# Optimization experiments

Hardware: AMD Instinct MI355X
Metric: run time of the kernel (lower is better)

## Reference

```python
import jax, jax.numpy as jnp
import numpy as np

B, T, D, M = 32, 2048, 128, 256   # batch, seq_len, pitch vocab d, encoder_output_dim m
FILTERS = [256, 256, 256]
TAU = 1.0                          # gumbel_temperature
ALPHA_INV = 1.0 / (D * 100)        # W init value: 1/alpha, alpha = d*100


def causal_dilated_conv(x, w, b, dilation):
    """x: [B,T,Cin], w: [K,Cin,Cout], causal left padding."""
    k = w.shape[0]
    pad = (k - 1) * dilation
    y = jax.lax.conv_general_dilated(
        x, w, window_strides=(1,), padding=[(pad, 0)],
        rhs_dilation=(dilation,),
        dimension_numbers=('NWC', 'WIO', 'NWC'))
    return y + b


def slow_weight_model(batch, w0, b0, w1, b1, w2, b2, w_out, b_out):
    """DilatedConvBlock: stack of causal dilated convs (relu) + 1x1 readout to m logits."""
    h = jax.nn.relu(causal_dilated_conv(batch, w0, b0, dilation=1))
    h = jax.nn.relu(causal_dilated_conv(h, w1, b1, dilation=2))
    h = jax.nn.relu(causal_dilated_conv(h, w2, b2, dilation=4))
    return causal_dilated_conv(h, w_out, b_out, dilation=1)  # [B,T,M] logits


def setup_inputs() -> dict:
    key = jax.random.key(0)
    ks = jax.random.split(key, 9)
    def glorot(k, shape):
        fan_in = np.prod(shape[:-1])
        return (jax.random.normal(k, shape, jnp.float32) / np.sqrt(fan_in)).astype(jnp.float32)
    return {
        'batch': jax.random.uniform(ks[0], (B, T, D), jnp.float32),
        'w0': glorot(ks[1], (2, D, FILTERS[0])), 'b0': jnp.zeros((FILTERS[0],), jnp.float32),
        'w1': glorot(ks[2], (2, FILTERS[0], FILTERS[1])), 'b1': jnp.zeros((FILTERS[1],), jnp.float32),
        'w2': glorot(ks[3], (2, FILTERS[1], FILTERS[2])), 'b2': jnp.zeros((FILTERS[2],), jnp.float32),
        'w_out': glorot(ks[4], (1, FILTERS[2], M)), 'b_out': jnp.zeros((M,), jnp.float32),
    }


def reference(batch, w0, b0, w1, b1, w2, b2, w_out, b_out):
    logits = slow_weight_model(batch, w0, b0, w1, b1, w2, b2, w_out, b_out)  # [B,T,M]
    # short_term_method == 'softmax_normalize_after'
    h_src = jax.nn.softmax(logits / TAU, axis=2)  # [B,T,M]
    s_tar = batch                                  # [B,T,D]
    W0 = jnp.full((B, M, D), ALPHA_INV, jnp.float32)

    def step(W, hs):
        h, s = hs                                              # [B,M], [B,D]
        num = jnp.einsum('bm,bmd->bd', h, W)                   # readout
        prob = num / jnp.sum(num, axis=-1, keepdims=True)      # normalize-after
        W_new = W + h[:, :, None] * s[:, None, :]              # outer-product fast-weight update
        return W_new, prob

    W_final, probs = jax.lax.scan(
        step, W0, (jnp.swapaxes(h_src, 0, 1), jnp.swapaxes(s_tar, 0, 1)))
    probs = jnp.swapaxes(probs, 0, 1)  # [B,T,D]
    return probs, W_final
```

## Files before the change

kernel.cpp:

```cpp
#include <hip/hip_runtime.h>

using u16 = unsigned short;
using u32 = unsigned int;
using short8 = __attribute__((ext_vector_type(8))) short;
using short4v = __attribute__((ext_vector_type(4))) short;
using bf16x8 = __attribute__((ext_vector_type(8))) __bf16;
using f32x4 = __attribute__((ext_vector_type(4))) float;

#define ALPHA_INV (1.0f / (128.0f * 100.0f))

__device__ __forceinline__ u32 swz(u32 off, u32 row) { return off ^ ((row & 7u) << 4); }

__device__ __forceinline__ u16 f2bf(float x) {
  u32 u = __float_as_uint(x);
  u32 r = u + 0x7fffu + ((u >> 16) & 1u);
  return (u16)(r >> 16);
}

__device__ __forceinline__ float bf2f(u16 x) {
  u32 u = ((u32)x) << 16;
  return __uint_as_float(u);
}

__device__ __forceinline__ f32x4 mfma(bf16x8 a, bf16x8 b, f32x4 c) {
  return __builtin_amdgcn_mfma_f32_16x16x32_bf16(a, b, c, 0, 0, 0);
}

__device__ __forceinline__ void gl16(const void* g, void* l) {
  __builtin_amdgcn_global_load_lds(
      (const __attribute__((address_space(1))) unsigned int*)g,
      (__attribute__((address_space(3))) unsigned int*)l, 16, 0, 0);
}

__global__ __launch_bounds__(256) void prep(
    const float* __restrict__ batch,
    const float* __restrict__ w0, const float* __restrict__ w1,
    const float* __restrict__ w2, const float* __restrict__ wo,
    u16* __restrict__ o0, u16* __restrict__ o1,
    u16* __restrict__ o2, u16* __restrict__ o3,
    u16* __restrict__ ST) {
  __shared__ u16 L[64 * 129];
  int blk = blockIdx.x;
  if (blk < 1536) {
    const float* w; u16* o; int cin;
    if (blk < 256)       { w = w0; o = o0; cin = 128; }
    else if (blk < 768)  { w = w1; o = o1; cin = 256; blk -= 256; }
    else if (blk < 1280) { w = w2; o = o2; cin = 256; blk -= 768; }
    else                 { w = wo; o = o3; cin = 256; blk -= 1280; }
    int idx = blk * 256 + threadIdx.x;
    int row = idx >> 8, n = idx & 255;
    int tap = row / cin, c = row - tap * cin;
    int kc = c >> 6, ci = c & 63;
    u32 sb = (u32)(ci * 2) ^ ((u32)(n & 7) << 4);
    o[((size_t)tap * 256 + n) * cin + kc * 64 + (sb >> 1)] = f2bf(w[idx]);
    return;
  }
  blk -= 1536;
  const int tid = threadIdx.x;
  const int t0 = (blk & 31) * 64;
  const int b = blk >> 5;
  const float* src = batch + ((size_t)b * 2048 + t0) * 128;
#pragma unroll
  for (int it = 0; it < 4; ++it) {
    int s = tid + it * 256;
    int t = s >> 4, c8 = s & 15;
    float4 v0 = *(const float4*)(src + t * 128 + c8 * 8);
    float4 v1 = *(const float4*)(src + t * 128 + c8 * 8 + 4);
    u16* p = &L[t * 129 + c8 * 8];
    p[0] = f2bf(v0.x); p[1] = f2bf(v0.y); p[2] = f2bf(v0.z); p[3] = f2bf(v0.w);
    p[4] = f2bf(v1.x); p[5] = f2bf(v1.y); p[6] = f2bf(v1.z); p[7] = f2bf(v1.w);
  }
  __syncthreads();
  u16* dst = ST + (size_t)b * 128 * 2048 + t0;
#pragma unroll
  for (int it = 0; it < 4; ++it) {
    int s = tid + it * 256;
    int oct = s & 7, d = s >> 3;
    short8 v;
#pragma unroll
    for (int j = 0; j < 8; ++j) v[j] = (short)L[(oct * 8 + j) * 129 + d];
    *(short8*)(dst + (size_t)d * 2048 + oct * 8) = v;
  }
}

__global__ __launch_bounds__(512) void conv_first(
    const float* __restrict__ in, const u16* __restrict__ wt,
    const float* __restrict__ bias, u16* __restrict__ out) {
  constexpr int CIN = 128, BN = 256;
  __shared__ alignas(16) u16 Al[128 * 64];
  __shared__ alignas(16) u16 Bl[256 * 64];

  const int tid = threadIdx.x;
  const int wid = tid >> 6, lane = tid & 63;
  const int wr = wid >> 2, wc = wid & 3;
  const int lg = lane >> 4, lq = lane & 15;
  const int row0 = blockIdx.x * 128;
  const int tloc0 = row0 & 2047;

  f32x4 acc[4][4];
#pragma unroll
  for (int i = 0; i < 4; ++i)
#pragma unroll
    for (int j = 0; j < 4; ++j) acc[i][j] = (f32x4)0.0f;

#pragma unroll
  for (int tap = 0; tap < 2; ++tap) {
    const int shift = 1 - tap;
#pragma unroll
    for (int kc = 0; kc < 2; ++kc) {
#pragma unroll
      for (int it = 0; it < 2; ++it) {
        int gi = tid + it * 512;
        int r = gi >> 3, cg = gi & 7;
        short8 v = (short8)0;
        if (!(tloc0 == 0 && r < shift)) {
          const float* src = in + (size_t)(row0 + r - shift) * CIN + kc * 64 + cg * 8;
          float4 a = *(const float4*)src;
          float4 b2 = *(const float4*)(src + 4);
          v[0] = (short)f2bf(a.x);  v[1] = (short)f2bf(a.y);
          v[2] = (short)f2bf(a.z);  v[3] = (short)f2bf(a.w);
          v[4] = (short)f2bf(b2.x); v[5] = (short)f2bf(b2.y);
          v[6] = (short)f2bf(b2.z); v[7] = (short)f2bf(b2.w);
        }
        *(short8*)((char*)Al + swz(r * 128 + cg * 16, (u32)(r - shift + 8))) = v;
      }
      {
        const u16* wtb = wt + ((size_t)(tap * 256)) * CIN + kc * 64;
#pragma unroll
        for (int it = 0; it < 4; ++it) {
          int gi = tid + it * 512;
          int n = gi >> 3, cg = gi & 7;
          gl16(wtb + (size_t)n * CIN + cg * 8, (char*)Bl + it * 8192 + wid * 1024);
        }
      }
      __syncthreads();
#pragma unroll
      for (int ks = 0; ks < 2; ++ks) {
        bf16x8 af[4], bfr[4];
#pragma unroll
        for (int mi = 0; mi < 4; ++mi) {
          int r = wr * 64 + mi * 16 + lq;
          af[mi] = *(const bf16x8*)((const char*)Al +
                                    swz(r * 128 + ks * 64 + lg * 16, (u32)(r - shift + 8)));
        }
#pragma unroll
        for (int ni = 0; ni < 4; ++ni) {
          int n = wc * 64 + ni * 16 + lq;
          bfr[ni] = *(const bf16x8*)((const char*)Bl + swz(n * 128 + ks * 64 + lg * 16, n));
        }
#pragma unroll
        for (int mi = 0; mi < 4; ++mi)
#pragma unroll
          for (int ni = 0; ni < 4; ++ni)
            acc[mi][ni] = mfma(af[mi], bfr[ni], acc[mi][ni]);
      }
      __syncthreads();
    }
  }

  float bcol[4];
#pragma unroll
  for (int ni = 0; ni < 4; ++ni) bcol[ni] = bias[wc * 64 + ni * 16 + lq];
#pragma unroll
  for (int mi = 0; mi < 4; ++mi)
#pragma unroll
    for (int ni = 0; ni < 4; ++ni)
#pragma unroll
      for (int rr = 0; rr < 4; ++rr) {
        float v = fmaxf(acc[mi][ni][rr] + bcol[ni], 0.0f);
        int row = row0 + wr * 64 + mi * 16 + lg * 4 + rr;
        int col = wc * 64 + ni * 16 + lq;
        int ci = col & 63;
        u32 sb = (u32)(ci * 2) ^ ((u32)(row & 7) << 4);
        out[(size_t)row * BN + wc * 64 + (sb >> 1)] = f2bf(v);
      }
}

template <int DIL>
__global__ __launch_bounds__(512) void conv_mid(
    const u16* __restrict__ in, const u16* __restrict__ wt,
    const float* __restrict__ bias, u16* __restrict__ out) {
  constexpr int CIN = 256, BN = 256;
  __shared__ alignas(16) u16 Al[3][136 * 64];
  __shared__ alignas(16) u16 Bl[3][256 * 64];

  const int tid = threadIdx.x;
  const int wid = tid >> 6, lane = tid & 63;
  const int wr = wid >> 2, wc = wid & 3;
  const int lg = lane >> 4, lq = lane & 15;
  const int row0 = blockIdx.x * 128;
  const int tloc0 = row0 & 2047;

  f32x4 acc[4][4];
#pragma unroll
  for (int i = 0; i < 4; ++i)
#pragma unroll
    for (int j = 0; j < 4; ++j) acc[i][j] = (f32x4)0.0f;

#define STAGE_MID(BUF, KC, TAP)                                                          \
  {                                                                                      \
    _Pragma("unroll") for (int p = 0; p < 2; ++p) {                                      \
      int gi = tid + p * 512;                                                            \
      gl16(in + (size_t)(row0 - DIL + (gi >> 3)) * CIN + (KC)*64 + (gi & 7) * 8,         \
           (char*)Al[BUF] + p * 8192 + wid * 1024);                                      \
    }                                                                                    \
    if (wid == 0)                                                                        \
      gl16(in + (size_t)(row0 - DIL + 128 + (lane >> 3)) * CIN + (KC)*64 + (lane & 7) * 8,\
           (char*)Al[BUF] + 16384);                                                      \
    const u16* wtb = wt + (size_t)(TAP)*256 * CIN + (KC)*64;                             \
    _Pragma("unroll") for (int p = 0; p < 4; ++p) {                                      \
      int gi = tid + p * 512;                                                            \
      gl16(wtb + (size_t)(gi >> 3) * CIN + (gi & 7) * 8,                                 \
           (char*)Bl[BUF] + p * 8192 + wid * 1024);                                      \
    }                                                                                    \
  }

  STAGE_MID(0, 0, 0);
  STAGE_MID(1, 0, 1);
  if (wid == 0)
    asm volatile("s_waitcnt vmcnt(7)" ::: "memory");
  else
    asm volatile("s_waitcnt vmcnt(6)" ::: "memory");
  __builtin_amdgcn_s_barrier();

#pragma unroll
  for (int it8 = 0; it8 < 8; ++it8) {
    const int buf = it8 % 3;
    const int tap = it8 & 1;
    if (tap == 0 && tloc0 == 0) {
      if (tid < DIL * 8) *(short8*)((char*)Al[buf] + tid * 16) = (short8)0;
      asm volatile("s_waitcnt lgkmcnt(0)" ::: "memory");
      __builtin_amdgcn_s_barrier();
    }
#pragma unroll
    for (int ks = 0; ks < 2; ++ks) {
      bf16x8 af[4], bfr[4];
#pragma unroll
      for (int mi = 0; mi < 4; ++mi) {
        int r = wr * 64 + mi * 16 + lq;
        if (tap == 0)
          af[mi] = *(const bf16x8*)((const char*)Al[buf] +
                                    swz(r * 128 + ks * 64 + lg * 16, (u32)(r - DIL + 8)));
        else
          af[mi] = *(const bf16x8*)((const char*)Al[buf] +
                                    swz((r + DIL) * 128 + ks * 64 + lg * 16, (u32)(r + 8)));
      }
#pragma unroll
      for (int ni = 0; ni < 4; ++ni) {
        int n = wc * 64 + ni * 16 + lq;
        bfr[ni] = *(const bf16x8*)((const char*)Bl[buf] + swz(n * 128 + ks * 64 + lg * 16, n));
      }
#pragma unroll
      for (int mi = 0; mi < 4; ++mi)
#pragma unroll
        for (int ni = 0; ni < 4; ++ni)
          acc[mi][ni] = mfma(af[mi], bfr[ni], acc[mi][ni]);
    }
    if (it8 < 6) {
      STAGE_MID((it8 + 2) % 3, (it8 + 2) >> 1, (it8 + 2) & 1);
    }
    if (it8 < 7) {
      if (it8 < 6) {
        if (wid == 0)
          asm volatile("s_waitcnt vmcnt(7)" ::: "memory");
        else
          asm volatile("s_waitcnt vmcnt(6)" ::: "memory");
      } else {
        asm volatile("s_waitcnt vmcnt(0)" ::: "memory");
      }
      __builtin_amdgcn_s_barrier();
    }
  }
#undef STAGE_MID

  float bcol[4];
#pragma unroll
  for (int ni = 0; ni < 4; ++ni) bcol[ni] = bias[wc * 64 + ni * 16 + lq];
#pragma unroll
  for (int mi = 0; mi < 4; ++mi)
#pragma unroll
    for (int ni = 0; ni < 4; ++ni)
#pragma unroll
      for (int rr = 0; rr < 4; ++rr) {
        float v = fmaxf(acc[mi][ni][rr] + bcol[ni], 0.0f);
        int row = row0 + wr * 64 + mi * 16 + lg * 4 + rr;
        int col = wc * 64 + ni * 16 + lq;
        int ci = col & 63;
        u32 sb = (u32)(ci * 2) ^ ((u32)(row & 7) << 4);
        out[(size_t)row * BN + wc * 64 + (sb >> 1)] = f2bf(v);
      }
}

__global__ __launch_bounds__(512) void conv_last(
    const u16* __restrict__ in, const u16* __restrict__ wt,
    const float* __restrict__ bias, u16* __restrict__ out) {
  constexpr int CIN = 256, BN = 256;
  __shared__ alignas(16) u16 Al[3][128 * 64];
  __shared__ alignas(16) u16 Bl[3][256 * 64];
  __shared__ float redA[4][128];
  __shared__ float redB[4][128];

  const int tid = threadIdx.x;
  const int wid = tid >> 6, lane = tid & 63;
  const int wr = wid >> 2, wc = wid & 3;
  const int lg = lane >> 4, lq = lane & 15;
  const int row0 = blockIdx.x * 128;

  f32x4 acc[4][4];
#pragma unroll
  for (int i = 0; i < 4; ++i)
#pragma unroll
    for (int j = 0; j < 4; ++j) acc[i][j] = (f32x4)0.0f;

#define STAGE_LAST(BUF, KC)                                                              \
  {                                                                                      \
    _Pragma("unroll") for (int p = 0; p < 2; ++p) {                                      \
      int gi = tid + p * 512;                                                            \
      gl16(in + (size_t)(row0 + (gi >> 3)) * CIN + (KC)*64 + (gi & 7) * 8,               \
           (char*)Al[BUF] + p * 8192 + wid * 1024);                                      \
    }                                                                                    \
    const u16* wtb = wt + (KC)*64;                                                       \
    _Pragma("unroll") for (int p = 0; p < 4; ++p) {                                      \
      int gi = tid + p * 512;                                                            \
      gl16(wtb + (size_t)(gi >> 3) * CIN + (gi & 7) * 8,                                 \
           (char*)Bl[BUF] + p * 8192 + wid * 1024);                                      \
    }                                                                                    \
  }

  STAGE_LAST(0, 0);
  STAGE_LAST(1, 1);
  asm volatile("s_waitcnt vmcnt(6)" ::: "memory");
  __builtin_amdgcn_s_barrier();

#pragma unroll
  for (int it4 = 0; it4 < 4; ++it4) {
    const int buf = it4 % 3;
#pragma unroll
    for (int ks = 0; ks < 2; ++ks) {
      bf16x8 af[4], bfr[4];
#pragma unroll
      for (int mi = 0; mi < 4; ++mi) {
        int r = wr * 64 + mi * 16 + lq;
        af[mi] = *(const bf16x8*)((const char*)Al[buf] +
                                  swz(r * 128 + ks * 64 + lg * 16, (u32)(r + 8)));
      }
#pragma unroll
      for (int ni = 0; ni < 4; ++ni) {
        int n = wc * 64 + ni * 16 + lq;
        bfr[ni] = *(const bf16x8*)((const char*)Bl[buf] + swz(n * 128 + ks * 64 + lg * 16, n));
      }
#pragma unroll
      for (int mi = 0; mi < 4; ++mi)
#pragma unroll
        for (int ni = 0; ni < 4; ++ni)
          acc[mi][ni] = mfma(af[mi], bfr[ni], acc[mi][ni]);
    }
    if (it4 < 2) {
      STAGE_LAST((it4 + 2) % 3, it4 + 2);
    }
    if (it4 < 3) {
      if (it4 < 2)
        asm volatile("s_waitcnt vmcnt(6)" ::: "memory");
      else
        asm volatile("s_waitcnt vmcnt(0)" ::: "memory");
      __builtin_amdgcn_s_barrier();
    }
  }
#undef STAGE_LAST
  __syncthreads();

  float bcol[4];
#pragma unroll
  for (int ni = 0; ni < 4; ++ni) bcol[ni] = bias[wc * 64 + ni * 16 + lq];
#pragma unroll
  for (int mi = 0; mi < 4; ++mi)
#pragma unroll
    for (int ni = 0; ni < 4; ++ni)
#pragma unroll
      for (int rr = 0; rr < 4; ++rr) acc[mi][ni][rr] += bcol[ni];

  float tmx[4][4];
#pragma unroll
  for (int mi = 0; mi < 4; ++mi)
#pragma unroll
    for (int rr = 0; rr < 4; ++rr) {
      float v = fmaxf(fmaxf(acc[mi][0][rr], acc[mi][1][rr]),
                      fmaxf(acc[mi][2][rr], acc[mi][3][rr]));
#pragma unroll
      for (int off = 1; off < 16; off <<= 1) v = fmaxf(v, __shfl_xor(v, off));
      if (lq == 0) redA[wc][wr * 64 + mi * 16 + lg * 4 + rr] = v;
    }
  __syncthreads();
#pragma unroll
  for (int mi = 0; mi < 4; ++mi)
#pragma unroll
    for (int rr = 0; rr < 4; ++rr) {
      int rb = wr * 64 + mi * 16 + lg * 4 + rr;
      tmx[mi][rr] = fmaxf(fmaxf(redA[0][rb], redA[1][rb]),
                          fmaxf(redA[2][rb], redA[3][rb]));
    }
#pragma unroll
  for (int mi = 0; mi < 4; ++mi)
#pragma unroll
    for (int rr = 0; rr < 4; ++rr) {
      float s = 0.0f;
#pragma unroll
      for (int ni = 0; ni < 4; ++ni) {
        float p = __expf(acc[mi][ni][rr] - tmx[mi][rr]);
        acc[mi][ni][rr] = p;
        s += p;
      }
#pragma unroll
      for (int off = 1; off < 16; off <<= 1) s += __shfl_xor(s, off);
      if (lq == 0) redB[wc][wr * 64 + mi * 16 + lg * 4 + rr] = s;
    }
  __syncthreads();
#pragma unroll
  for (int mi = 0; mi < 4; ++mi)
#pragma unroll
    for (int rr = 0; rr < 4; ++rr) {
      int rb = wr * 64 + mi * 16 + lg * 4 + rr;
      float inv = 1.0f / (redB[0][rb] + redB[1][rb] + redB[2][rb] + redB[3][rb]);
      int row = row0 + rb;
#pragma unroll
      for (int ni = 0; ni < 4; ++ni) {
        int col = wc * 64 + ni * 16 + lq;
        out[(size_t)row * BN + col] = f2bf(acc[mi][ni][rr] * inv);
      }
    }
}

__global__ __launch_bounds__(512) void gchunk(
    const u16* __restrict__ H, const u16* __restrict__ ST,
    u16* __restrict__ G0, u16* __restrict__ G1) {
  constexpr int M = 256, T = 2048;
  __shared__ alignas(16) u16 Hl[128 * 128];
  __shared__ alignas(16) u16 Sl[128 * 128];
  const int tid = threadIdx.x;
  const int wid = tid >> 6, lane = tid & 63;
  const int dg = wid >> 2, mg = wid & 3;
  const int lg = lane >> 4, lq = lane & 15;
  const int b = blockIdx.x, mh = blockIdx.y, j = blockIdx.z;
  u16* G = (mh == 0 ? G0 : G1);

#pragma unroll
  for (int it = 0; it < 4; ++it) {
    int s = tid + it * 512;
    int t = s >> 4, c8 = s & 15;
    short8 v = *(const short8*)(H + ((size_t)b * T + j * 128 + t) * M + mh * 128 + c8 * 8);
#pragma unroll
    for (int jj = 0; jj < 8; ++jj) {
      int ml = c8 * 8 + jj;
      *(u16*)((char*)Hl + swz(ml * 256 + t * 2, ml)) = (u16)v[jj];
    }
  }
#pragma unroll
  for (int it = 0; it < 4; ++it) {
    int s = tid + it * 512;
    int d = s >> 4, c8 = s & 15;
    *(short8*)((char*)Sl + swz(d * 256 + c8 * 16, d)) =
        *(const short8*)(ST + ((size_t)b * 128 + d) * T + j * 128 + c8 * 8);
  }
  __syncthreads();

  f32x4 acc[4][2];
#pragma unroll
  for (int di = 0; di < 4; ++di)
#pragma unroll
    for (int mi = 0; mi < 2; ++mi) acc[di][mi] = (f32x4)0.0f;

#pragma unroll
  for (int ks = 0; ks < 4; ++ks) {
    bf16x8 sfrag[4];
#pragma unroll
    for (int di = 0; di < 4; ++di) {
      int d = dg * 64 + di * 16 + lq;
      sfrag[di] = *(const bf16x8*)((const char*)Sl + swz(d * 256 + ks * 64 + lg * 16, d));
    }
#pragma unroll
    for (int mi = 0; mi < 2; ++mi) {
      int ml = mg * 32 + mi * 16 + lq;
      bf16x8 hfrag =
          *(const bf16x8*)((const char*)Hl + swz(ml * 256 + ks * 64 + lg * 16, ml));
#pragma unroll
      for (int di = 0; di < 4; ++di) acc[di][mi] = mfma(sfrag[di], hfrag, acc[di][mi]);
    }
  }

  u16* Gj = G + (((size_t)b * 16 + j) << 14);
#pragma unroll
  for (int di = 0; di < 4; ++di)
#pragma unroll
    for (int mi = 0; mi < 2; ++mi)
#pragma unroll
      for (int rr = 0; rr < 4; ++rr) {
        int d = dg * 64 + di * 16 + lg * 4 + rr;
        int ml = mg * 32 + mi * 16 + lq;
        Gj[d * 128 + ml] = f2bf(acc[di][mi][rr]);
      }
}

__global__ __launch_bounds__(256) void prefix_wfin(
    u16* __restrict__ G0, u16* __restrict__ G1, float* __restrict__ wfin) {
  __shared__ float Wl[16][132];
  const int b = blockIdx.x, mh = blockIdx.y, ds = blockIdx.z;
  u16* G = mh ? G1 : G0;
  const int tid = threadIdx.x;
  const int mo = tid & 15, dg = tid >> 4;
  const int d = ds * 16 + dg;
  size_t base = (((size_t)b * 16) << 14) + d * 128 + mo * 8;
  float acc[8];
#pragma unroll
  for (int k = 0; k < 8; ++k) acc[k] = ALPHA_INV;
  for (int j = 0; j < 16; ++j) {
    u16* p = G + base + ((size_t)j << 14);
    short8 g = *(short8*)p;
    short8 c;
#pragma unroll
    for (int k = 0; k < 8; ++k) c[k] = (short)f2bf(acc[k]);
    *(short8*)p = c;
#pragma unroll
    for (int k = 0; k < 8; ++k) acc[k] += bf2f((u16)g[k]);
  }
#pragma unroll
  for (int k = 0; k < 8; ++k) Wl[dg][mo * 8 + k] = acc[k];
  __syncthreads();
  const int ml = tid >> 1, dq = tid & 1;
  const int dl0 = dq * 8;
  float* dst = wfin + ((size_t)b * 256 + mh * 128 + ml) * 128 + ds * 16 + dl0;
  float4 v0 = make_float4(Wl[dl0][ml], Wl[dl0 + 1][ml], Wl[dl0 + 2][ml], Wl[dl0 + 3][ml]);
  float4 v1 = make_float4(Wl[dl0 + 4][ml], Wl[dl0 + 5][ml], Wl[dl0 + 6][ml], Wl[dl0 + 7][ml]);
  *(float4*)dst = v0;
  *(float4*)(dst + 4) = v1;
}

__global__ __launch_bounds__(512) void attn_chunk(
    const u16* __restrict__ H, const u16* __restrict__ ST,
    const u16* __restrict__ C0, const u16* __restrict__ C1,
    float* __restrict__ out) {
  constexpr int M = 256, D = 128, T = 2048;
  __shared__ alignas(16) u16 Hi[128 * 256];
  __shared__ alignas(16) u16 Sl[128 * 128];
  __shared__ alignas(16) u16 Ct[128 * 128];

  const int tid = threadIdx.x;
  const int wid = tid >> 6, lane = tid & 63;
  const int lg = lane >> 4, lq = lane & 15;
  const int b = blockIdx.x, i = blockIdx.y;
  const size_t hrow0 = (size_t)b * T + i * 128;
  const size_t coff = ((size_t)b * 16 + i) * (128 * 128);

  bf16x8 aq[8];
  {
    const u16* qrow = H + (hrow0 + wid * 16 + lq) * M;
#pragma unroll
    for (int ks = 0; ks < 8; ++ks) aq[ks] = *(const bf16x8*)(qrow + ks * 32 + lg * 8);
  }

  short8 ct1r[4];
#pragma unroll
  for (int it = 0; it < 4; ++it) {
    int s = tid + it * 512;
    int d = s >> 4, c8 = s & 15;
    ct1r[it] = *(const short8*)(C1 + coff + d * 128 + c8 * 8);
  }

  {
    int r = wid * 16 + lq;
#pragma unroll
    for (int ks = 0; ks < 8; ++ks)
      *(short8*)((char*)Hi + swz(r * 512 + ks * 64 + lg * 16, r)) =
          __builtin_bit_cast(short8, aq[ks]);
  }
#pragma unroll
  for (int it = 0; it < 4; ++it) {
    int s = tid + it * 512;
    int d = s >> 4, c8 = s & 15;
    *(short8*)((char*)Sl + swz(d * 256 + c8 * 16, d)) =
        *(const short8*)(ST + ((size_t)b * D + d) * T + i * 128 + c8 * 8);
  }
#pragma unroll
  for (int it = 0; it < 4; ++it) {
    int s = tid + it * 512;
    int d = s >> 4, c8 = s & 15;
    *(short8*)((char*)Ct + swz(d * 256 + c8 * 16, d)) = *(const short8*)(C0 + coff + d * 128 + c8 * 8);
  }
  __syncthreads();

  f32x4 accO[8];
#pragma unroll
  for (int df = 0; df < 8; ++df) accO[df] = (f32x4)0.0f;
#pragma unroll
  for (int ks = 0; ks < 4; ++ks)
#pragma unroll
    for (int df = 0; df < 8; ++df) {
      int d = df * 16 + lq;
      bf16x8 bf = *(const bf16x8*)((const char*)Ct + swz(d * 256 + ks * 64 + lg * 16, d));
      accO[df] = mfma(aq[ks], bf, accO[df]);
    }
  f32x4 accP[8];
#pragma unroll
  for (int cf = 0; cf < 8; ++cf) accP[cf] = (f32x4)0.0f;
#pragma unroll
  for (int ks = 0; ks < 8; ++ks)
#pragma unroll
    for (int cf = 0; cf < 8; ++cf) {
      int tt = cf * 16 + lq;
      bf16x8 bf = *(const bf16x8*)((const char*)Hi + swz(tt * 512 + ks * 64 + lg * 16, tt));
      accP[cf] = mfma(aq[ks], bf, accP[cf]);
    }
  __syncthreads();

#pragma unroll
  for (int it = 0; it < 4; ++it) {
    int s = tid + it * 512;
    int d = s >> 4, c8 = s & 15;
    *(short8*)((char*)Ct + swz(d * 256 + c8 * 16, d)) = ct1r[it];
  }
  char* Pw = (char*)Hi + wid * 4096;
#pragma unroll
  for (int cf = 0; cf < 8; ++cf)
#pragma unroll
    for (int rr = 0; rr < 4; ++rr) {
      int ql = lg * 4 + rr;
      int tl = cf * 16 + lq;
      float v = accP[cf][rr];
      if (tl >= wid * 16 + ql) v = 0.0f;
      *(u16*)(Pw + swz(ql * 256 + tl * 2, ql)) = f2bf(v);
    }
  __syncthreads();

#pragma unroll
  for (int ks = 0; ks < 4; ++ks)
#pragma unroll
    for (int df = 0; df < 8; ++df) {
      int d = df * 16 + lq;
      bf16x8 bf = *(const bf16x8*)((const char*)Ct + swz(d * 256 + ks * 64 + lg * 16, d));
      accO[df] = mfma(aq[4 + ks], bf, accO[df]);
    }
#pragma unroll
  for (int ks = 0; ks < 4; ++ks) {
    bf16x8 a = *(const bf16x8*)(Pw + swz(lq * 256 + ks * 64 + lg * 16, lq));
#pragma unroll
    for (int df = 0; df < 8; ++df) {
      int d = df * 16 + lq;
      bf16x8 bf = *(const bf16x8*)((const char*)Sl + swz(d * 256 + ks * 64 + lg * 16, d));
      accO[df] = mfma(a, bf, accO[df]);
    }
  }

#pragma unroll
  for (int rr = 0; rr < 4; ++rr) {
    float ssum = 0.0f;
#pragma unroll
    for (int df = 0; df < 8; ++df) ssum += accO[df][rr];
#pragma unroll
    for (int off = 1; off < 16; off <<= 1) ssum += __shfl_xor(ssum, off);
    float inv = 1.0f / ssum;
    size_t row = hrow0 + wid * 16 + lg * 4 + rr;
#pragma unroll
    for (int df = 0; df < 8; ++df)
      out[row * D + df * 16 + lq] = accO[df][rr] * inv;
  }
}

extern "C" void kernel_launch(void* const* d_in, const int* in_sizes, int n_in,
                              void* d_out, int out_size, void* d_ws, size_t ws_size,
                              hipStream_t stream) {
  const float* batch = (const float*)d_in[0];
  const float* w0 = (const float*)d_in[1];
  const float* b0 = (const float*)d_in[2];
  const float* w1 = (const float*)d_in[3];
  const float* b1 = (const float*)d_in[4];
  const float* w2 = (const float*)d_in[5];
  const float* b2 = (const float*)d_in[6];
  const float* wo = (const float*)d_in[7];
  const float* bo = (const float*)d_in[8];

  const size_t SZ_S = 16777216;
  const size_t SZ_BUF = 33554432;
  const size_t ST_OFF = 88080384;
  const size_t NEED = ST_OFF + SZ_S;
  if (ws_size < NEED) return;

  char* ws = (char*)d_ws;
  u16* bufA = (u16*)(ws + SZ_S);
  u16* bufB = (u16*)(ws + SZ_S + SZ_BUF);
  u16* Wt0 = (u16*)(ws + SZ_S + 2 * SZ_BUF);
  u16* Wt1 = Wt0 + 2 * 256 * 128;
  u16* Wt2 = Wt1 + 2 * 256 * 256;
  u16* Wt3 = Wt2 + 2 * 256 * 256;
  u16* ST = (u16*)(ws + ST_OFF);
  u16* G0 = (u16*)ws;
  u16* G1 = (u16*)(ws + 2 * SZ_S);
  float* probs = (float*)d_out;
  float* wfin = probs + (size_t)32 * 2048 * 128;

  prep<<<2560, 256, 0, stream>>>(batch, w0, w1, w2, wo, Wt0, Wt1, Wt2, Wt3, ST);

  conv_first<<<512, 512, 0, stream>>>(batch, Wt0, b0, bufA);
  conv_mid<2><<<512, 512, 0, stream>>>(bufA, Wt1, b1, bufB);
  conv_mid<4><<<512, 512, 0, stream>>>(bufB, Wt2, b2, bufA);
  conv_last<<<512, 512, 0, stream>>>(bufA, Wt3, bo, bufB);

  gchunk<<<dim3(32, 2, 16), 512, 0, stream>>>(bufB, ST, G0, G1);
  prefix_wfin<<<dim3(32, 2, 8), 256, 0, stream>>>(G0, G1, wfin);
  attn_chunk<<<dim3(32, 16), 512, 0, stream>>>(bufB, ST, G0, G1, probs);
}
```

Before: 174.5 us.

## Triple-buffer first conv layer LDS staging to overlap loads with MFMA

Rewrites the conv_first K loop as a 3-stage software pipeline. Weight tiles are prefetched two steps ahead with async global-to-LDS loads, and the next activation tile is converted and written while the current one feeds the MFMAs. Explicit vmcnt waits replace one of the two barriers per step. This costs three times the LDS (about 144 KB), which may cut occupancy or exceed the LDS limit, and only the first conv kernel changes.

```diff
diff --git a/kernel.cpp b/kernel.cpp
--- a/kernel.cpp
+++ b/kernel.cpp
@@ -87,8 +87,8 @@
     const float* __restrict__ in, const u16* __restrict__ wt,
     const float* __restrict__ bias, u16* __restrict__ out) {
   constexpr int CIN = 128, BN = 256;
-  __shared__ alignas(16) u16 Al[128 * 64];
-  __shared__ alignas(16) u16 Bl[256 * 64];
+  __shared__ alignas(16) u16 Al[3][128 * 64];
+  __shared__ alignas(16) u16 Bl[3][256 * 64];
 
   const int tid = threadIdx.x;
   const int wid = tid >> 6, lane = tid & 63;
@@ -103,60 +103,80 @@
 #pragma unroll
     for (int j = 0; j < 4; ++j) acc[i][j] = (f32x4)0.0f;
 
-#pragma unroll
-  for (int tap = 0; tap < 2; ++tap) {
-    const int shift = 1 - tap;
-#pragma unroll
-    for (int kc = 0; kc < 2; ++kc) {
-#pragma unroll
-      for (int it = 0; it < 2; ++it) {
-        int gi = tid + it * 512;
-        int r = gi >> 3, cg = gi & 7;
-        short8 v = (short8)0;
-        if (!(tloc0 == 0 && r < shift)) {
-          const float* src = in + (size_t)(row0 + r - shift) * CIN + kc * 64 + cg * 8;
-          float4 a = *(const float4*)src;
-          float4 b2 = *(const float4*)(src + 4);
-          v[0] = (short)f2bf(a.x);  v[1] = (short)f2bf(a.y);
-          v[2] = (short)f2bf(a.z);  v[3] = (short)f2bf(a.w);
-          v[4] = (short)f2bf(b2.x); v[5] = (short)f2bf(b2.y);
-          v[6] = (short)f2bf(b2.z); v[7] = (short)f2bf(b2.w);
-        }
-        *(short8*)((char*)Al + swz(r * 128 + cg * 16, (u32)(r - shift + 8))) = v;
-      }
-      {
-        const u16* wtb = wt + ((size_t)(tap * 256)) * CIN + kc * 64;
-#pragma unroll
-        for (int it = 0; it < 4; ++it) {
-          int gi = tid + it * 512;
-          int n = gi >> 3, cg = gi & 7;
-          gl16(wtb + (size_t)n * CIN + cg * 8, (char*)Bl + it * 8192 + wid * 1024);
-        }
-      }
-      __syncthreads();
-#pragma unroll
-      for (int ks = 0; ks < 2; ++ks) {
-        bf16x8 af[4], bfr[4];
-#pragma unroll
-        for (int mi = 0; mi < 4; ++mi) {
-          int r = wr * 64 + mi * 16 + lq;
-          af[mi] = *(const bf16x8*)((const char*)Al +
-                                    swz(r * 128 + ks * 64 + lg * 16, (u32)(r - shift + 8)));
-        }
-#pragma unroll
-        for (int ni = 0; ni < 4; ++ni) {
-          int n = wc * 64 + ni * 16 + lq;
-          bfr[ni] = *(const bf16x8*)((const char*)Bl + swz(n * 128 + ks * 64 + lg * 16, n));
-        }
-#pragma unroll
-        for (int mi = 0; mi < 4; ++mi)
-#pragma unroll
-          for (int ni = 0; ni < 4; ++ni)
-            acc[mi][ni] = mfma(af[mi], bfr[ni], acc[mi][ni]);
-      }
-      __syncthreads();
-    }
-  }
+#define WRITE_A(BUF, T)                                                                  \
+  {                                                                                      \
+    const int tap_ = (T) >> 1, kc_ = (T) & 1, shift_ = 1 - tap_;                         \
+    _Pragma("unroll") for (int it = 0; it < 2; ++it) {                                   \
+      int gi = tid + it * 512;                                                           \
+      int r = gi >> 3, cg = gi & 7;                                                      \
+      short8 v = (short8)0;                                                              \
+      if (!(tloc0 == 0 && r < shift_)) {                                                 \
+        const float* src = in + (size_t)(row0 + r - shift_) * CIN + kc_ * 64 + cg * 8;   \
+        float4 a = *(const float4*)src;                                                  \
+        float4 b2 = *(const float4*)(src + 4);                                           \
+        v[0] = (short)f2bf(a.x);  v[1] = (short)f2bf(a.y);                               \
+        v[2] = (short)f2bf(a.z);  v[3] = (short)f2bf(a.w);                               \
+        v[4] = (short)f2bf(b2.x); v[5] = (short)f2bf(b2.y);                              \
+        v[6] = (short)f2bf(b2.z); v[7] = (short)f2bf(b2.w);                              \
+      }                                                                                  \
+      *(short8*)((char*)Al[BUF] + swz(r * 128 + cg * 16, (u32)(r - shift_ + 8))) = v;    \
+    }                                                                                    \
+  }
+
+#define STAGE_B1(BUF, T)                                                                 \
+  {                                                                                      \
+    const int tap_ = (T) >> 1, kc_ = (T) & 1;                                            \
+    const u16* wtb = wt + (size_t)(tap_ * 256) * CIN + kc_ * 64;                         \
+    _Pragma("unroll") for (int p = 0; p < 4; ++p) {                                      \
+      int gi = tid + p * 512;                                                            \
+      gl16(wtb + (size_t)(gi >> 3) * CIN + (gi & 7) * 8,                                 \
+           (char*)Bl[BUF] + p * 8192 + wid * 1024);                                      \
+    }                                                                                    \
+  }
+
+  STAGE_B1(0, 0);
+  STAGE_B1(1, 1);
+  WRITE_A(0, 0);
+  asm volatile("s_waitcnt vmcnt(0) lgkmcnt(0)" ::: "memory");
+  __builtin_amdgcn_s_barrier();
+
+#pragma unroll
+  for (int t = 0; t < 4; ++t) {
+    const int buf = t % 3;
+    const int shift = 1 - (t >> 1);
+#pragma unroll
+    for (int ks = 0; ks < 2; ++ks) {
+      bf16x8 af[4], bfr[4];
+#pragma unroll
+      for (int mi = 0; mi < 4; ++mi) {
+        int r = wr * 64 + mi * 16 + lq;
+        af[mi] = *(const bf16x8*)((const char*)Al[buf] +
+                                  swz(r * 128 + ks * 64 + lg * 16, (u32)(r - shift + 8)));
+      }
+#pragma unroll
+      for (int ni = 0; ni < 4; ++ni) {
+        int n = wc * 64 + ni * 16 + lq;
+        bfr[ni] = *(const bf16x8*)((const char*)Bl[buf] + swz(n * 128 + ks * 64 + lg * 16, n));
+      }
+#pragma unroll
+      for (int mi = 0; mi < 4; ++mi)
+#pragma unroll
+        for (int ni = 0; ni < 4; ++ni)
+          acc[mi][ni] = mfma(af[mi], bfr[ni], acc[mi][ni]);
+    }
+    if (t < 3) {
+      WRITE_A((t + 1) % 3, t + 1);
+      if (t < 2) {
+        STAGE_B1((t + 2) % 3, t + 2);
+        asm volatile("s_waitcnt vmcnt(4) lgkmcnt(0)" ::: "memory");
+      } else {
+        asm volatile("s_waitcnt vmcnt(0) lgkmcnt(0)" ::: "memory");
+      }
+      __builtin_amdgcn_s_barrier();
+    }
+  }
+#undef WRITE_A
+#undef STAGE_B1
 
   float bcol[4];
 #pragma unroll
```

Measured after the change: 173.0 us (median of 2 runs). About the same (-0.9%).
